# Optimization experiments

Hardware: AMD Instinct MI355X
Metric: run time of the kernel (lower is better)

The kernel has to match this reference:

```python
import jax, jax.numpy as jnp
import numpy as np
from jax.scipy.linalg import expm

B = 16384
K = 64          # number of subgroups
M = 6           # mat_dim per subgroup (subgroup_size = 36)
NUM_ACTIONS = 16


def setup_inputs() -> dict:
    key = jax.random.key(0)
    k1, k2, k3, k4 = jax.random.split(key, 4)
    group_feats = jax.random.normal(k1, (B, K * M * M), dtype=jnp.float32)
    act = jax.random.randint(k2, (B,), 0, NUM_ACTIONS)
    act_params = jax.random.normal(k3, (NUM_ACTIONS, K), dtype=jnp.float32) * 0.001
    lie_alg_basis = jax.random.normal(k4, (K, M, M), dtype=jnp.float32)
    return {"group_feats": group_feats, "act": act,
            "act_params": act_params, "lie_alg_basis": lie_alg_basis}


def reference(group_feats, act, act_params, lie_alg_basis):
    # apply_act: act_repr = blockdiag_k expm(a_{bk} * (L_k - L_k^T)); out = act_repr @ blockdiag(group_feats)
    sel = act_params[act]                                   # [B, K]  (index_select on act_params)
    skew = lie_alg_basis - jnp.swapaxes(lie_alg_basis, -2, -1)  # [K, M, M]
    lie_alg = sel[:, :, None, None] * skew[None]            # [B, K, M, M]
    # batched matrix exponential over all B*K small blocks
    lie_group = jax.vmap(expm)(lie_alg.reshape(-1, M, M)).reshape(B, K, M, M)
    gf_mat = group_feats.reshape(B, K, M, M)                # to_group_matrix (block-diag blocks)
    # block-diagonal matmul == full dense matmul since off-diagonal blocks are zero
    post = jnp.einsum('bkij,bkjl->bkil', lie_group, gf_mat)
    return post.reshape(B, K * M * M)                       # to_group_feats
```

## Files before the change

kernel.cpp:

```cpp
#include <hip/hip_runtime.h>
#include <stdint.h>

#define BATCH 16384
#define KSUB 64
#define MDIM 6
#define MM 36
#define NACT 16
#define F4PB 9
#define WGT 64
#define LDSPITCH 37

typedef float f32x4 __attribute__((ext_vector_type(4)));

__global__ void expm_table_kernel(const float* __restrict__ act_params,
                                  const float* __restrict__ basis,
                                  float* __restrict__ Rtab)
{
    int gid = blockIdx.x * blockDim.x + threadIdx.x;
    if (gid >= NACT * KSUB) return;
    int a = gid / KSUB;
    int k = gid - a * KSUB;

    float L[MM];
#pragma unroll
    for (int i = 0; i < MM; ++i) L[i] = basis[k * MM + i];
    float p = act_params[a * KSUB + k];

    float A[MM];
#pragma unroll
    for (int i = 0; i < MDIM; ++i)
#pragma unroll
        for (int j = 0; j < MDIM; ++j)
            A[i * MDIM + j] = p * (L[i * MDIM + j] - L[j * MDIM + i]);

    float E[MM], T[MM];
#pragma unroll
    for (int i = 0; i < MM; ++i) { E[i] = 0.f; T[i] = 0.f; }
#pragma unroll
    for (int i = 0; i < MDIM; ++i) { E[i * MDIM + i] = 1.f; T[i * MDIM + i] = 1.f; }

    for (int n = 1; n <= 10; ++n) {
        float Tn[MM];
        float inv = 1.0f / (float)n;
#pragma unroll
        for (int i = 0; i < MDIM; ++i)
#pragma unroll
            for (int l = 0; l < MDIM; ++l) {
                float s = 0.f;
#pragma unroll
                for (int j = 0; j < MDIM; ++j)
                    s += A[i * MDIM + j] * T[j * MDIM + l];
                Tn[i * MDIM + l] = s * inv;
            }
#pragma unroll
        for (int i = 0; i < MM; ++i) { T[i] = Tn[i]; E[i] += Tn[i]; }
    }
#pragma unroll
    for (int i = 0; i < MM; ++i) Rtab[gid * MM + i] = E[i];
}

__global__ __launch_bounds__(WGT, 4) void apply_kernel(
    const f32x4* __restrict__ gf4,
    const int* __restrict__ act,
    const float* __restrict__ Rtab,
    f32x4* __restrict__ out4)
{
    __shared__ float lds[WGT * LDSPITCH];
    const int tid = threadIdx.x;
    const int b = blockIdx.x;
    const size_t base4 = (size_t)b * (WGT * F4PB);

    const int a = act[b];
    const f32x4* R4 = (const f32x4*)(Rtab + (size_t)((a << 6) + tid) * MM);
    f32x4 rv[F4PB];
#pragma unroll
    for (int q = 0; q < F4PB; ++q) rv[q] = R4[q];

#pragma unroll
    for (int i = 0; i < F4PB; ++i) {
        int p4 = tid + (i << 6);
        f32x4 v = __builtin_nontemporal_load(&gf4[base4 + p4]);
        int n = p4 / F4PB;
        int j = (p4 - n * F4PB) * 4;
        float* row = &lds[n * LDSPITCH + j];
        row[0] = v.x; row[1] = v.y; row[2] = v.z; row[3] = v.w;
    }
    __syncthreads();

    float G[MM];
#pragma unroll
    for (int j = 0; j < MM; ++j) G[j] = lds[tid * LDSPITCH + j];

    float Rv[MM];
#pragma unroll
    for (int q = 0; q < F4PB; ++q) {
        Rv[4 * q + 0] = rv[q].x; Rv[4 * q + 1] = rv[q].y;
        Rv[4 * q + 2] = rv[q].z; Rv[4 * q + 3] = rv[q].w;
    }
    float O[MM];
#pragma unroll
    for (int i = 0; i < MM; ++i) O[i] = 0.f;
#pragma unroll
    for (int j = 0; j < MDIM; ++j)
#pragma unroll
        for (int i = 0; i < MDIM; ++i) {
            float r = Rv[i * MDIM + j];
#pragma unroll
            for (int l = 0; l < MDIM; ++l)
                O[i * MDIM + l] = fmaf(r, G[j * MDIM + l], O[i * MDIM + l]);
        }

    __syncthreads();
#pragma unroll
    for (int j = 0; j < MM; ++j) lds[tid * LDSPITCH + j] = O[j];
    __syncthreads();

#pragma unroll
    for (int i = 0; i < F4PB; ++i) {
        int p4 = tid + (i << 6);
        int n = p4 / F4PB;
        int j = (p4 - n * F4PB) * 4;
        const float* row = &lds[n * LDSPITCH + j];
        f32x4 v;
        v.x = row[0]; v.y = row[1]; v.z = row[2]; v.w = row[3];
        __builtin_nontemporal_store(v, &out4[base4 + p4]);
    }
}

extern "C" void kernel_launch(void* const* d_in, const int* in_sizes, int n_in,
                              void* d_out, int out_size, void* d_ws, size_t ws_size,
                              hipStream_t stream) {
    const float* gf    = (const float*)d_in[0];
    const int*   act   = (const int*)d_in[1];
    const float* ap    = (const float*)d_in[2];
    const float* basis = (const float*)d_in[3];

    float* Rtab = (float*)d_ws;

    expm_table_kernel<<<16, 64, 0, stream>>>(ap, basis, Rtab);

    apply_kernel<<<BATCH, WGT, 0, stream>>>((const f32x4*)gf, act, Rtab,
                                            (f32x4*)d_out);
}
```

Before: 266.6 us.

## Load group features straight into LDS and use vectorized LDS accesses

The apply kernel now streams input tiles from global memory directly into shared memory with global_load_lds, so the data no longer passes through registers with scalar scatter stores. The padded scalar LDS layout is replaced by an unpadded f32x4 array that is read as f32x2 pairs and written back as f32x4, which cuts LDS instruction count but may bring bank conflicts from the 36-float row stride. One barrier is removed because each thread overwrites only its own row, and the first FMA pass becomes a plain multiply.

New measurement: 275.1 us. +3.2%, slower.

```diff
diff --git a/kernel.cpp b/kernel.cpp
--- a/kernel.cpp
+++ b/kernel.cpp
@@ -8,9 +8,9 @@
 #define NACT 16
 #define F4PB 9
 #define WGT 64
-#define LDSPITCH 37
 
 typedef float f32x4 __attribute__((ext_vector_type(4)));
+typedef float f32x2 __attribute__((ext_vector_type(2)));
 
 __global__ void expm_table_kernel(const float* __restrict__ act_params,
                                   const float* __restrict__ basis,
@@ -65,65 +65,75 @@
     const float* __restrict__ Rtab,
     f32x4* __restrict__ out4)
 {
-    __shared__ float lds[WGT * LDSPITCH];
+    __shared__ f32x4 lds4[WGT * F4PB];
     const int tid = threadIdx.x;
     const int b = blockIdx.x;
     const size_t base4 = (size_t)b * (WGT * F4PB);
 
+#pragma unroll
+    for (int i = 0; i < F4PB; ++i) {
+        __builtin_amdgcn_global_load_lds(
+            (const __attribute__((address_space(1))) uint32_t*)(gf4 + base4 + (i << 6) + tid),
+            (__attribute__((address_space(3))) uint32_t*)(&lds4[i << 6]),
+            16, 0, 0);
+    }
+
     const int a = act[b];
     const f32x4* R4 = (const f32x4*)(Rtab + (size_t)((a << 6) + tid) * MM);
-    f32x4 rv[F4PB];
+    float R[MM];
 #pragma unroll
-    for (int q = 0; q < F4PB; ++q) rv[q] = R4[q];
+    for (int q = 0; q < F4PB; ++q) {
+        f32x4 rv = R4[q];
+        R[4 * q + 0] = rv.x; R[4 * q + 1] = rv.y;
+        R[4 * q + 2] = rv.z; R[4 * q + 3] = rv.w;
+    }
 
-#pragma unroll
-    for (int i = 0; i < F4PB; ++i) {
-        int p4 = tid + (i << 6);
-        f32x4 v = __builtin_nontemporal_load(&gf4[base4 + p4]);
-        int n = p4 / F4PB;
-        int j = (p4 - n * F4PB) * 4;
-        float* row = &lds[n * LDSPITCH + j];
-        row[0] = v.x; row[1] = v.y; row[2] = v.z; row[3] = v.w;
-    }
     __syncthreads();
 
-    float G[MM];
+    const f32x2* grow = (const f32x2*)(&lds4[tid * F4PB]);
+    float O[MM];
 #pragma unroll
-    for (int j = 0; j < MM; ++j) G[j] = lds[tid * LDSPITCH + j];
+    for (int j = 0; j < MDIM; ++j) {
+        f32x2 ga = grow[3 * j + 0];
+        f32x2 gb = grow[3 * j + 1];
+        f32x2 gc = grow[3 * j + 2];
+        float g0 = ga.x, g1 = ga.y, g2 = gb.x, g3 = gb.y, g4 = gc.x, g5 = gc.y;
+        if (j == 0) {
+#pragma unroll
+            for (int i = 0; i < MDIM; ++i) {
+                float r = R[i * MDIM + 0];
+                O[i * MDIM + 0] = r * g0; O[i * MDIM + 1] = r * g1;
+                O[i * MDIM + 2] = r * g2; O[i * MDIM + 3] = r * g3;
+                O[i * MDIM + 4] = r * g4; O[i * MDIM + 5] = r * g5;
+            }
+        } else {
+#pragma unroll
+            for (int i = 0; i < MDIM; ++i) {
+                float r = R[i * MDIM + j];
+                O[i * MDIM + 0] = fmaf(r, g0, O[i * MDIM + 0]);
+                O[i * MDIM + 1] = fmaf(r, g1, O[i * MDIM + 1]);
+                O[i * MDIM + 2] = fmaf(r, g2, O[i * MDIM + 2]);
+                O[i * MDIM + 3] = fmaf(r, g3, O[i * MDIM + 3]);
+                O[i * MDIM + 4] = fmaf(r, g4, O[i * MDIM + 4]);
+                O[i * MDIM + 5] = fmaf(r, g5, O[i * MDIM + 5]);
+            }
+        }
+    }
 
-    float Rv[MM];
+    f32x4* orow = (f32x4*)(&lds4[tid * F4PB]);
 #pragma unroll
     for (int q = 0; q < F4PB; ++q) {
-        Rv[4 * q + 0] = rv[q].x; Rv[4 * q + 1] = rv[q].y;
-        Rv[4 * q + 2] = rv[q].z; Rv[4 * q + 3] = rv[q].w;
+        f32x4 v;
+        v.x = O[4 * q + 0]; v.y = O[4 * q + 1];
+        v.z = O[4 * q + 2]; v.w = O[4 * q + 3];
+        orow[q] = v;
     }
-    float O[MM];
-#pragma unroll
-    for (int i = 0; i < MM; ++i) O[i] = 0.f;
-#pragma unroll
-    for (int j = 0; j < MDIM; ++j)
-#pragma unroll
-        for (int i = 0; i < MDIM; ++i) {
-            float r = Rv[i * MDIM + j];
-#pragma unroll
-            for (int l = 0; l < MDIM; ++l)
-                O[i * MDIM + l] = fmaf(r, G[j * MDIM + l], O[i * MDIM + l]);
-        }
-
-    __syncthreads();
-#pragma unroll
-    for (int j = 0; j < MM; ++j) lds[tid * LDSPITCH + j] = O[j];
     __syncthreads();
 
 #pragma unroll
     for (int i = 0; i < F4PB; ++i) {
-        int p4 = tid + (i << 6);
-        int n = p4 / F4PB;
-        int j = (p4 - n * F4PB) * 4;
-        const float* row = &lds[n * LDSPITCH + j];
-        f32x4 v;
-        v.x = row[0]; v.y = row[1]; v.z = row[2]; v.w = row[3];
-        __builtin_nontemporal_store(v, &out4[base4 + p4]);
+        int p4 = (i << 6) + tid;
+        __builtin_nontemporal_store(lds4[p4], &out4[base4 + p4]);
     }
 }
 
```
